# Kernel tuning notes

Measured on AMD Instinct MI355X. Metric: run time of the kernel, lower is better.

The kernel has to match this reference:

```python
import jax, jax.numpy as jnp
import numpy as np

B, TASK, LQ, D = 16, 80, 1024, 768
HH, HD, P, NL = 12, 64, 4, 1
HF, WF = 64, 64
LIN = HF * WF
EPS = 1e-6


def _ln(x, w, b):
    mu = jnp.mean(x, -1, keepdims=True)
    var = jnp.mean(jnp.square(x - mu), -1, keepdims=True)
    return (x - mu) * jax.lax.rsqrt(var + EPS) * w + b


def _bilinear(value_l, loc_l, Hl, Wl):
    # value_l: [B, HH, S, HD]; loc_l: [B, LQ, HH, P, 2] in [0,1]
    # replicates F.grid_sample(align_corners=False, padding_mode='zeros')
    b, hh, s, hd = value_l.shape
    lq, p = loc_l.shape[1], loc_l.shape[3]
    x = loc_l[..., 0] * Wl - 0.5
    y = loc_l[..., 1] * Hl - 0.5
    x0 = jnp.floor(x)
    y0 = jnp.floor(y)
    out = jnp.zeros((b, hh, lq, p, hd), value_l.dtype)
    for dx in (0, 1):
        for dy in (0, 1):
            xc = x0 + dx
            yc = y0 + dy
            w = (1.0 - jnp.abs(x - xc)) * (1.0 - jnp.abs(y - yc))
            valid = (xc >= 0) & (xc <= Wl - 1) & (yc >= 0) & (yc <= Hl - 1)
            w = jnp.where(valid, w, 0.0)
            xi = jnp.clip(xc, 0, Wl - 1).astype(jnp.int32)
            yi = jnp.clip(yc, 0, Hl - 1).astype(jnp.int32)
            lin = (yi * Wl + xi).transpose(0, 2, 1, 3).reshape(b, hh, lq * p, 1)
            v = jnp.take_along_axis(value_l, lin, axis=2).reshape(b, hh, lq, p, hd)
            out = out + v * w.transpose(0, 2, 1, 3)[..., None]
    return out


def _forward(query, reference_points, feat, spatial_shapes, level_start_index,
             qn_w, qn_b, fn_w, fn_b, gamma,
             W_off, b_off, W_attw, b_attw, W_val, b_val, W_out, b_out):
    ss = np.asarray(spatial_shapes)
    lsi = np.asarray(level_start_index)
    tt = query[:, :TASK]
    q = query[:, TASK:]
    bq, lq, _ = q.shape
    qn = _ln(q, qn_w, qn_b)
    fn = _ln(feat, fn_w, fn_b)
    # value projection: [B, Lin, D] -> [B, HH, Lin, HD]
    value = (fn @ W_val + b_val).reshape(bq, -1, HH, HD).transpose(0, 2, 1, 3)
    off = (qn @ W_off + b_off).reshape(bq, lq, HH, NL, P, 2)
    aw = (qn @ W_attw + b_attw).reshape(bq, lq, HH, NL * P)
    aw = jax.nn.softmax(aw, axis=-1).reshape(bq, lq, HH, NL, P)
    # offset normalizer is [W, H] per level
    norm = jnp.stack([ss[:, 1].astype(jnp.float32), ss[:, 0].astype(jnp.float32)], -1)
    loc = reference_points[:, :, None, :, None, :] + off / norm[None, None, None, :, None, :]
    out = jnp.zeros((bq, lq, HH, HD), query.dtype)
    for l in range(ss.shape[0]):
        Hl, Wl = int(ss[l, 0]), int(ss[l, 1])
        st = int(lsi[l])
        vl = value[:, :, st:st + Hl * Wl]
        sampled = _bilinear(vl, loc[:, :, :, l], Hl, Wl)  # [B,HH,LQ,P,HD]
        out = out + jnp.einsum('bhqpd,bqhp->bqhd', sampled, aw[:, :, :, l])
    attn = out.reshape(bq, lq, HH * HD) @ W_out + b_out
    q = q + gamma * attn
    return jnp.concatenate([tt, q], axis=1)


def setup_inputs():
    key = jax.random.key(0)
    ks = jax.random.split(key, 10)
    s = 0.02
    return {
        "query": jax.random.normal(ks[0], (B, TASK + LQ, D), jnp.float32),
        "reference_points": jax.random.uniform(ks[1], (B, LQ, NL, 2), dtype=jnp.float32),
        "feat": jax.random.normal(ks[2], (B, LIN, D), jnp.float32),
        "spatial_shapes": jnp.array([[HF, WF]], jnp.int32),
        "level_start_index": jnp.array([0], jnp.int32),
        "qn_w": jnp.ones((D,), jnp.float32),
        "qn_b": jnp.zeros((D,), jnp.float32),
        "fn_w": jnp.ones((D,), jnp.float32),
        "fn_b": jnp.zeros((D,), jnp.float32),
        "gamma": 0.1 * jax.random.normal(ks[3], (D,), jnp.float32),
        "W_off": s * jax.random.normal(ks[4], (D, HH * NL * P * 2), jnp.float32),
        "b_off": s * jax.random.normal(ks[5], (HH * NL * P * 2,), jnp.float32),
        "W_attw": s * jax.random.normal(ks[6], (D, HH * NL * P), jnp.float32),
        "b_attw": s * jax.random.normal(ks[7], (HH * NL * P,), jnp.float32),
        "W_val": s * jax.random.normal(ks[8], (D, D), jnp.float32),
        "b_val": jnp.zeros((D,), jnp.float32),
        "W_out": s * jax.random.normal(ks[9], (D, D), jnp.float32),
        "b_out": jnp.zeros((D,), jnp.float32),
    }


def reference(query, reference_points, feat, spatial_shapes, level_start_index, qn_w, qn_b, fn_w, fn_b, gamma, W_off, b_off, W_attw, b_attw, W_val, b_val, W_out, b_out):
    return _forward(query, reference_points, feat, spatial_shapes, level_start_index,
                    qn_w, qn_b, fn_w, fn_b, gamma,
                    W_off, b_off, W_attw, b_attw, W_val, b_val, W_out, b_out)
```

## Files before the change

### kernel.cpp

```cpp
#include <hip/hip_runtime.h>
#include <hip/hip_bf16.h>

using bf16 = __hip_bfloat16;
typedef __attribute__((ext_vector_type(8))) short short8;
typedef __attribute__((ext_vector_type(4))) short short4v;
typedef __attribute__((ext_vector_type(4))) float floatx4;

#define B_    16
#define TASK_ 80
#define LQ_   1024
#define D_    768
#define HH_   12
#define HD_   64
#define LIN_  4096
#define MQ_   (B_*LQ_)
#define MF_   (B_*LIN_)
#define QR_   (TASK_+LQ_)

static constexpr size_t OFF_VAL = 0;
static constexpr size_t OFF_FN  = OFF_VAL + (size_t)MF_*D_*2;
static constexpr size_t OFF_QN  = OFF_FN  + (size_t)MF_*D_*2;
static constexpr size_t OFF_OA  = OFF_QN  + (size_t)MQ_*D_*2;
static constexpr size_t OFF_WVT = OFF_OA  + (size_t)MQ_*144*4;
static constexpr size_t OFF_WOT = OFF_WVT + (size_t)D_*D_*2;
static constexpr size_t OFF_WCT = OFF_WOT + (size_t)D_*D_*2;

__device__ __forceinline__ void async16(const void* g, void* l) {
  __builtin_amdgcn_global_load_lds((const __attribute__((address_space(1))) void*)g,
                                   (__attribute__((address_space(3))) void*)l, 16, 0, 0);
}

__global__ __launch_bounds__(256) void k_wln(const float* __restrict__ Wv, const float* __restrict__ Wo,
                                             const float* __restrict__ Woff, const float* __restrict__ Wat,
                                             bf16* __restrict__ WvT, bf16* __restrict__ WoT,
                                             bf16* __restrict__ WcT,
                                             const float* __restrict__ query, const float* __restrict__ feat,
                                             const float* __restrict__ qw, const float* __restrict__ qb,
                                             const float* __restrict__ fw, const float* __restrict__ fb,
                                             bf16* __restrict__ qn, bf16* __restrict__ fn) {
  __shared__ float t[64][65];
  int bid = blockIdx.x;
  if (bid < 288) {
    const float* W = (bid < 144) ? Wv : Wo;
    bf16* WT = (bid < 144) ? WvT : WoT;
    int lb = (bid < 144) ? bid : bid - 144;
    int bx = lb % 12, by = lb / 12;
    int n0 = bx*64, k0 = by*64;
    int col = threadIdx.x & 63, rg = threadIdx.x >> 6;
    #pragma unroll
    for (int i=0;i<16;++i) { int row = i*4+rg; t[row][col] = W[(size_t)(k0+row)*D_ + n0+col]; }
    __syncthreads();
    #pragma unroll
    for (int i=0;i<16;++i) { int row = i*4+rg; WT[(size_t)(n0+row)*D_ + k0+col] = __float2bfloat16(t[col][row]); }
    return;
  }
  if (bid < 1056) {
    int idx = (bid-288)*256 + threadIdx.x;
    int j = idx / D_, k = idx - j*D_;
    float v = 0.f;
    if (j < 96)       v = Woff[(size_t)k*96 + j];
    else if (j < 144) v = Wat[(size_t)k*48 + (j-96)];
    WcT[idx] = __float2bfloat16(v);
    return;
  }
  int r = (bid-1056)*4 + (threadIdx.x>>6);
  int lane = threadIdx.x & 63;
  const float* src; const float* w; const float* bia; bf16* dst;
  if (r < MQ_) {
    int bat = r >> 10, rr = r & 1023;
    src = query + ((size_t)bat*QR_ + TASK_ + rr)*D_;
    w = qw; bia = qb; dst = qn + (size_t)r*D_;
  } else {
    int fr = r - MQ_;
    src = feat + (size_t)fr*D_;
    w = fw; bia = fb; dst = fn + (size_t)fr*D_;
  }
  float4 v[3];
  #pragma unroll
  for (int j=0;j<3;++j) v[j] = ((const float4*)src)[lane + 64*j];
  float s = 0.f, s2 = 0.f;
  #pragma unroll
  for (int j=0;j<3;++j) {
    s  += v[j].x + v[j].y + v[j].z + v[j].w;
    s2 += v[j].x*v[j].x + v[j].y*v[j].y + v[j].z*v[j].z + v[j].w*v[j].w;
  }
  #pragma unroll
  for (int o=32;o>0;o>>=1){ s += __shfl_xor(s,o); s2 += __shfl_xor(s2,o); }
  float mu  = s*(1.f/D_);
  float var = s2*(1.f/D_) - mu*mu;
  float rstd = rsqrtf(var + 1e-6f);
  #pragma unroll
  for (int j=0;j<3;++j) {
    float4 ww = ((const float4*)w)[lane + 64*j];
    float4 bb = ((const float4*)bia)[lane + 64*j];
    short4v o4;
    o4[0] = (short)__bfloat16_as_ushort(__float2bfloat16((v[j].x-mu)*rstd*ww.x + bb.x));
    o4[1] = (short)__bfloat16_as_ushort(__float2bfloat16((v[j].y-mu)*rstd*ww.y + bb.y));
    o4[2] = (short)__bfloat16_as_ushort(__float2bfloat16((v[j].z-mu)*rstd*ww.z + bb.z));
    o4[3] = (short)__bfloat16_as_ushort(__float2bfloat16((v[j].w-mu)*rstd*ww.w + bb.w));
    *(short4v*)(dst + 4*(lane + 64*j)) = o4;
  }
}

template<int MODE>
__global__ __launch_bounds__(512, 2) void k_gemm256(const bf16* __restrict__ A, const bf16* __restrict__ BT,
                                                    const float* __restrict__ bias0, void* __restrict__ outp,
                                                    const float* __restrict__ query, const float* __restrict__ gamma) {
  __shared__ char lds[98304];
  const int K = D_;
  const int tid = threadIdx.x, wid = tid>>6, lane = tid&63;
  const int nwg = gridDim.x*gridDim.y;
  const int d = blockIdx.y*gridDim.x + blockIdx.x;
  const int logical = (d & 7)*(nwg>>3) + (d>>3);
  const int bm = (logical/3)*256, bn = (logical%3)*256;
  const int wm = wid>>2, wn = wid&3;
  const int srow = tid>>2;
  const int sslot = ((tid&3) ^ ((tid>>3)&3))*8;
  const bf16* gA0 = A  + (size_t)(bm + srow)*K + sslot;
  const bf16* gA1 = A  + (size_t)(bm + 128 + srow)*K + sslot;
  const bf16* gB0 = BT + (size_t)(bn + srow)*K + sslot;
  const bf16* gB1 = BT + (size_t)(bn + 128 + srow)*K + sslot;
  const int dstbase = (tid>>6)<<10;
  const int rb = (lane&15)*64 + ((((lane>>4) ^ ((lane>>1)&3)))<<4);
  floatx4 acc[8][4] = {};
  auto stageAll = [&](int k0, char* buf) {
    async16(gA0+k0, buf + dstbase);
    async16(gA1+k0, buf + 8192 + dstbase);
    async16(gB0+k0, buf + 16384 + dstbase);
    async16(gB1+k0, buf + 24576 + dstbase);
  };
  stageAll(0,  lds);
  stageAll(32, lds + 32768);
  const int NT = K >> 5;
  int cur = 0, nxt = 2;
  for (int k = 0; k < NT; ++k) {
    if (k < NT-1) asm volatile("s_waitcnt vmcnt(4)" ::: "memory");
    else          asm volatile("s_waitcnt vmcnt(0)" ::: "memory");
    __builtin_amdgcn_s_barrier();
    __builtin_amdgcn_sched_barrier(0);
    const int kk = (k+2)*32;
    const bool pf = (k+2 < NT);
    const char* lA = lds + cur*32768;
    const char* lB = lA + 16384;
    char* bufn = lds + nxt*32768;
    short8 af[8], bfr[4];
    if (pf) async16(gA0+kk, bufn + dstbase);
    #pragma unroll
    for (int i=0;i<4;++i) af[i] = *(const short8*)(lA + (wm*128 + i*16)*64 + rb);
    #pragma unroll
    for (int i=0;i<2;++i) bfr[i] = *(const short8*)(lB + (wn*64 + i*16)*64 + rb);
    __builtin_amdgcn_s_barrier();
    __builtin_amdgcn_s_setprio(1);
    #pragma unroll
    for (int mi=0;mi<4;++mi)
      #pragma unroll
      for (int ni=0;ni<2;++ni)
        acc[mi][ni] = __builtin_amdgcn_mfma_f32_16x16x32_bf16(af[mi], bfr[ni], acc[mi][ni], 0, 0, 0);
    __builtin_amdgcn_s_setprio(0);
    __builtin_amdgcn_s_barrier();
    __builtin_amdgcn_sched_barrier(0);
    if (pf) async16(gA1+kk, bufn + 8192 + dstbase);
    #pragma unroll
    for (int i=2;i<4;++i) bfr[i] = *(const short8*)(lB + (wn*64 + i*16)*64 + rb);
    __builtin_amdgcn_s_barrier();
    __builtin_amdgcn_s_setprio(1);
    #pragma unroll
    for (int mi=0;mi<4;++mi)
      #pragma unroll
      for (int ni=2;ni<4;++ni)
        acc[mi][ni] = __builtin_amdgcn_mfma_f32_16x16x32_bf16(af[mi], bfr[ni], acc[mi][ni], 0, 0, 0);
    __builtin_amdgcn_s_setprio(0);
    __builtin_amdgcn_s_barrier();
    __builtin_amdgcn_sched_barrier(0);
    if (pf) async16(gB0+kk, bufn + 16384 + dstbase);
    #pragma unroll
    for (int i=4;i<8;++i) af[i] = *(const short8*)(lA + (wm*128 + i*16)*64 + rb);
    __builtin_amdgcn_s_barrier();
    __builtin_amdgcn_s_setprio(1);
    #pragma unroll
    for (int mi=4;mi<8;++mi)
      #pragma unroll
      for (int ni=0;ni<2;++ni)
        acc[mi][ni] = __builtin_amdgcn_mfma_f32_16x16x32_bf16(af[mi], bfr[ni], acc[mi][ni], 0, 0, 0);
    __builtin_amdgcn_s_setprio(0);
    __builtin_amdgcn_s_barrier();
    __builtin_amdgcn_sched_barrier(0);
    if (pf) async16(gB1+kk, bufn + 24576 + dstbase);
    __builtin_amdgcn_s_barrier();
    __builtin_amdgcn_s_setprio(1);
    #pragma unroll
    for (int mi=4;mi<8;++mi)
      #pragma unroll
      for (int ni=2;ni<4;++ni)
        acc[mi][ni] = __builtin_amdgcn_mfma_f32_16x16x32_bf16(af[mi], bfr[ni], acc[mi][ni], 0, 0, 0);
    __builtin_amdgcn_s_setprio(0);
    __builtin_amdgcn_sched_barrier(0);
    cur = (cur==2) ? 0 : cur+1;
    nxt = (nxt==2) ? 0 : nxt+1;
  }
  const int rowb = (lane>>4)*4, col = lane&15;
  #pragma unroll
  for (int mi=0;mi<8;++mi) {
    #pragma unroll
    for (int ni=0;ni<4;++ni) {
      const int gn = bn + wn*64 + ni*16 + col;
      const float bv = bias0[gn];
      #pragma unroll
      for (int r=0;r<4;++r) {
        const int gm = bm + wm*128 + mi*16 + rowb + r;
        if constexpr (MODE==0) {
          const int h = gn >> 6, hd = gn & 63;
          const int b = gm >> 12, pix = gm & 4095;
          ((bf16*)outp)[(((size_t)(b*HH_+h)*LIN_ + pix)<<6) + hd] = __float2bfloat16(acc[mi][ni][r] + bv);
        } else {
          const int bq = gm >> 10, lq = gm & 1023;
          size_t idx = ((size_t)bq*QR_ + TASK_ + lq)*D_ + gn;
          ((float*)outp)[idx] = query[idx] + gamma[gn]*(acc[mi][ni][r] + bv);
        }
      }
    }
  }
}

__global__ __launch_bounds__(256) void k_gemm1(const bf16* __restrict__ A, const bf16* __restrict__ BT,
                                               int K,
                                               const float* __restrict__ bias0, const float* __restrict__ bias1,
                                               float* __restrict__ outp) {
  __shared__ char lds[49152];
  const int tid = threadIdx.x, wid = tid>>6, lane = tid&63;
  const int nwg = gridDim.x*gridDim.y, ny = gridDim.y;
  const int d = blockIdx.y*gridDim.x + blockIdx.x;
  const int logical = (d & 7)*(nwg>>3) + (d>>3);
  const int bm = (logical/ny)*128, bn = (logical%ny)*128;
  const int wr = wid>>1, wc = wid&1;
  const int c0 = wid*2, c1 = c0+1;
  const int sr0 = c0*16 + (lane>>2), sr1 = sr0+16;
  const int skb = (((lane&3) ^ ((lane>>3)&3)))*8;
  const bf16* ga0 = A  + (size_t)(bm+sr0)*K + skb;
  const bf16* ga1 = A  + (size_t)(bm+sr1)*K + skb;
  const bf16* gb0 = BT + (size_t)(bn+sr0)*K + skb;
  const bf16* gb1 = BT + (size_t)(bn+sr1)*K + skb;
  const int rb = (lane&15)*64 + ((((lane>>4) ^ ((lane>>1)&3)))<<4);
  floatx4 acc[4][4] = {};
  auto stage = [&](int k0, char* buf) {
    char* dA = buf; char* dB = buf + 8192;
    async16(ga0+k0, dA + c0*1024); async16(ga1+k0, dA + c1*1024);
    async16(gb0+k0, dB + c0*1024); async16(gb1+k0, dB + c1*1024);
  };
  stage(0,  lds);
  stage(32, lds + 16384);
  const int NT = K >> 5;
  int cur = 0, nxt = 2;
  for (int k = 0; k < NT; ++k) {
    if (k < NT-1) asm volatile("s_waitcnt vmcnt(4)" ::: "memory");
    else          asm volatile("s_waitcnt vmcnt(0)" ::: "memory");
    __builtin_amdgcn_s_barrier();
    __builtin_amdgcn_sched_barrier(0);
    if (k + 2 < NT) stage((k+2)*32, lds + nxt*16384);
    const char* ldsA = lds + cur*16384; const char* ldsB = ldsA + 8192;
    short8 af[4], bfr[4];
    #pragma unroll
    for (int i=0;i<4;++i) {
      af[i]  = *(const short8*)(ldsA + (wr*64 + i*16)*64 + rb);
      bfr[i] = *(const short8*)(ldsB + (wc*64 + i*16)*64 + rb);
    }
    #pragma unroll
    for (int mi=0;mi<4;++mi)
      #pragma unroll
      for (int ni=0;ni<4;++ni)
        acc[mi][ni] = __builtin_amdgcn_mfma_f32_16x16x32_bf16(af[mi], bfr[ni], acc[mi][ni], 0, 0, 0);
    cur = (cur==2) ? 0 : cur+1;
    nxt = (nxt==2) ? 0 : nxt+1;
  }
  const int rowb = (lane>>4)*4, col = lane&15;
  #pragma unroll
  for (int mi=0;mi<4;++mi) {
    #pragma unroll
    for (int ni=0;ni<4;++ni) {
      const int gn = bn + wc*64 + ni*16 + col;
      #pragma unroll
      for (int r=0;r<4;++r) {
        const int gm = bm + wr*64 + mi*16 + rowb + r;
        float v = acc[mi][ni][r];
        if (gn < 144) {
          v += (gn < 96) ? bias0[gn] : bias1[gn-96];
          outp[(size_t)gm*144 + gn] = v;
        }
      }
    }
  }
}

__global__ __launch_bounds__(256) void k_prep(const float* __restrict__ oa_all,
                                              const float* __restrict__ refp,
                                              float2* __restrict__ prep,
                                              const float* __restrict__ query, float* __restrict__ out) {
  int idx = blockIdx.x*256 + threadIdx.x;
  int p = idx & 3, mh = idx >> 2;
  int h = mh % HH_, m = mh / HH_;
  const float* oa = oa_all + (size_t)m*144;
  float l0 = oa[96+h*4+0], l1 = oa[96+h*4+1], l2 = oa[96+h*4+2], l3 = oa[96+h*4+3];
  float mx = fmaxf(fmaxf(l0,l1), fmaxf(l2,l3));
  float e0 = expf(l0-mx), e1 = expf(l1-mx), e2 = expf(l2-mx), e3 = expf(l3-mx);
  float inv = 1.f/(e0+e1+e2+e3);
  float ep = (p==0)?e0:(p==1)?e1:(p==2)?e2:e3;
  float awp = ep*inv;
  float x = refp[(size_t)m*2+0]*64.f - 0.5f + oa[h*8+p*2+0];
  float y = refp[(size_t)m*2+1]*64.f - 0.5f + oa[h*8+p*2+1];
  float x0f = floorf(x), y0f = floorf(y);
  int ix = (int)x0f, iy = (int)y0f;
  float fx = x-x0f, fy = y-y0f;
  float wx[2] = {1.f-fx, fx}, wy[2] = {1.f-fy, fy};
  float2 e[4];
  #pragma unroll
  for (int c=0;c<4;++c) {
    int dx = c&1, dy = c>>1;
    int xc = ix+dx, yc = iy+dy;
    bool valid = ((unsigned)xc < 64u) && ((unsigned)yc < 64u);
    float w = valid ? awp*wx[dx]*wy[dy] : 0.f;
    int xi = min(max(xc,0),63), yi = min(max(yc,0),63);
    e[c].x = w;
    e[c].y = __int_as_float(yi*64+xi);
  }
  float2* dst = prep + (size_t)mh*16 + p*4;
  *(float4*)(dst)   = make_float4(e[0].x, e[0].y, e[1].x, e[1].y);
  *(float4*)(dst+2) = make_float4(e[2].x, e[2].y, e[3].x, e[3].y);
  if (blockIdx.x < 960) {
    int ci = blockIdx.x*256 + threadIdx.x;
    const int perb = TASK_*D_/4;
    int b = ci / perb, r = ci - b*perb;
    const float4* s = (const float4*)(query + (size_t)b*QR_*D_) + r;
    float4* dd = (float4*)(out + (size_t)b*QR_*D_) + r;
    *dd = *s;
  }
}

__global__ __launch_bounds__(256) void k_sample(const float2* __restrict__ prep,
                                                const bf16* __restrict__ value,
                                                bf16* __restrict__ sampout) {
  int g  = blockIdx.x*8 + (threadIdx.x>>5);
  int l  = threadIdx.x & 31;
  int c8 = l >> 2, p = l & 3;
  int h = g % HH_, m = g / HH_;
  int b = m >> 10;
  const float2* pb = prep + (size_t)g*16 + p*4;
  float4 e01 = *(const float4*)(pb);
  float4 e23 = *(const float4*)(pb+2);
  const bf16* vb = value + (((size_t)(b*HH_+h))<<18) + (c8<<3);
  float a[8] = {};
  float wv[4]  = {e01.x, e01.z, e23.x, e23.z};
  int   pix[4] = {__float_as_int(e01.y), __float_as_int(e01.w),
                  __float_as_int(e23.y), __float_as_int(e23.w)};
  #pragma unroll
  for (int c=0;c<4;++c) {
    short8 v = *(const short8*)(vb + ((size_t)pix[c]<<6));
    float w = wv[c];
    #pragma unroll
    for (int j=0;j<8;++j)
      a[j] += w*__uint_as_float(((unsigned)(unsigned short)v[j])<<16);
  }
  #pragma unroll
  for (int j=0;j<8;++j) { a[j] += __shfl_xor(a[j],1); a[j] += __shfl_xor(a[j],2); }
  if (p == 0) {
    short8 o;
    #pragma unroll
    for (int j=0;j<8;++j)
      o[j] = (short)__bfloat16_as_ushort(__float2bfloat16(a[j]));
    *(short8*)(sampout + (size_t)m*D_ + h*64 + c8*8) = o;
  }
}

extern "C" void kernel_launch(void* const* d_in, const int* in_sizes, int n_in,
                              void* d_out, int out_size, void* d_ws, size_t ws_size,
                              hipStream_t stream) {
  (void)in_sizes; (void)n_in; (void)out_size; (void)ws_size;
  const float* query = (const float*)d_in[0];
  const float* refp  = (const float*)d_in[1];
  const float* feat  = (const float*)d_in[2];
  const float* qn_w  = (const float*)d_in[5];
  const float* qn_b  = (const float*)d_in[6];
  const float* fn_w  = (const float*)d_in[7];
  const float* fn_b  = (const float*)d_in[8];
  const float* gamma = (const float*)d_in[9];
  const float* W_off = (const float*)d_in[10];
  const float* b_off = (const float*)d_in[11];
  const float* W_attw= (const float*)d_in[12];
  const float* b_attw= (const float*)d_in[13];
  const float* W_val = (const float*)d_in[14];
  const float* b_val = (const float*)d_in[15];
  const float* W_out = (const float*)d_in[16];
  const float* b_out = (const float*)d_in[17];
  char*  ws  = (char*)d_ws;
  float* out = (float*)d_out;

  bf16*   wsVal  = (bf16*)(ws + OFF_VAL);
  bf16*   wsFn   = (bf16*)(ws + OFF_FN);
  bf16*   wsQn   = (bf16*)(ws + OFF_QN);
  float*  wsOA   = (float*)(ws + OFF_OA);
  bf16*   wsWvT  = (bf16*)(ws + OFF_WVT);
  bf16*   wsWoT  = (bf16*)(ws + OFF_WOT);
  bf16*   wsWcT  = (bf16*)(ws + OFF_WCT);
  float2* wsPrep = (float2*)(ws + OFF_QN);
  bf16*   wsSamp = wsFn;

  k_wln<<<1056 + (MQ_+MF_)/4, 256, 0, stream>>>(W_val, W_out, W_off, W_attw, wsWvT, wsWoT, wsWcT,
                                                query, feat, qn_w, qn_b, fn_w, fn_b, wsQn, wsFn);
  k_gemm1<<<dim3(MQ_/128, 2), 256, 0, stream>>>(wsQn, wsWcT, D_, b_off, b_attw, wsOA);
  k_prep<<<(MQ_*HH_*4)/256, 256, 0, stream>>>(wsOA, refp, wsPrep, query, out);
  k_gemm256<0><<<dim3(MF_/256, 3), 512, 0, stream>>>(wsFn, wsWvT, b_val, wsVal, nullptr, nullptr);
  k_sample<<<(MQ_*HH_)/8, 256, 0, stream>>>(wsPrep, wsVal, wsSamp);
  k_gemm256<2><<<dim3(MQ_/256, 3), 512, 0, stream>>>(wsSamp, wsWoT, b_out, out, query, gamma);
}
```

Measured before the change: 276.2 us.

## Fuse offset/attention GEMM with sampling prep and pack prep data as bf16/u16

New measurement: 269.2 us. 1.03x faster.

```diff
diff --git a/kernel.cpp b/kernel.cpp
--- a/kernel.cpp
+++ b/kernel.cpp
@@ -17,13 +17,13 @@
 #define MF_   (B_*LIN_)
 #define QR_   (TASK_+LQ_)
 
-static constexpr size_t OFF_VAL = 0;
-static constexpr size_t OFF_FN  = OFF_VAL + (size_t)MF_*D_*2;
-static constexpr size_t OFF_QN  = OFF_FN  + (size_t)MF_*D_*2;
-static constexpr size_t OFF_OA  = OFF_QN  + (size_t)MQ_*D_*2;
-static constexpr size_t OFF_WVT = OFF_OA  + (size_t)MQ_*144*4;
-static constexpr size_t OFF_WOT = OFF_WVT + (size_t)D_*D_*2;
-static constexpr size_t OFF_WCT = OFF_WOT + (size_t)D_*D_*2;
+static constexpr size_t OFF_VAL  = 0;
+static constexpr size_t OFF_FN   = OFF_VAL + (size_t)MF_*D_*2;
+static constexpr size_t OFF_QN   = OFF_FN  + (size_t)MF_*D_*2;
+static constexpr size_t OFF_PREP = OFF_QN  + (size_t)MQ_*D_*2;
+static constexpr size_t OFF_WVT  = OFF_PREP + (size_t)MQ_*HH_*64;
+static constexpr size_t OFF_WOT  = OFF_WVT + (size_t)D_*D_*2;
+static constexpr size_t OFF_WCT  = OFF_WOT + (size_t)D_*D_*2;
 
 __device__ __forceinline__ void async16(const void* g, void* l) {
   __builtin_amdgcn_global_load_lds((const __attribute__((address_space(1))) void*)g,
@@ -99,6 +99,118 @@
     o4[2] = (short)__bfloat16_as_ushort(__float2bfloat16((v[j].z-mu)*rstd*ww.z + bb.z));
     o4[3] = (short)__bfloat16_as_ushort(__float2bfloat16((v[j].w-mu)*rstd*ww.w + bb.w));
     *(short4v*)(dst + 4*(lane + 64*j)) = o4;
+  }
+}
+
+__global__ __launch_bounds__(256) void k_offprep(const bf16* __restrict__ A, const bf16* __restrict__ BT,
+                                                 const float* __restrict__ b_off, const float* __restrict__ b_attw,
+                                                 const float* __restrict__ refp, char* __restrict__ prepc,
+                                                 const float* __restrict__ query, float* __restrict__ out) {
+  __shared__ char lds[49152];
+  const int tid = threadIdx.x, wid = tid>>6, lane = tid&63;
+  const int bm = blockIdx.x*64;
+  const int K = D_;
+  const int srow = tid>>2;
+  const int skb = ((tid&3) ^ ((tid>>3)&3))*8;
+  const bf16* gA  = A  + (size_t)(bm + srow)*K + skb;
+  const bf16* gB  = BT + (size_t)srow*K + skb;
+  const int dstbase = wid<<10;
+  const int rb = (lane&15)*64 + ((((lane>>4) ^ ((lane>>1)&3)))<<4);
+  floatx4 acc[4][3] = {};
+  auto stage = [&](int k0, char* buf) {
+    async16(gA + k0,                 buf + dstbase);
+    async16(gB + k0,                 buf + 4096  + dstbase);
+    async16(gB + (size_t)64*K + k0,  buf + 8192  + dstbase);
+    async16(gB + (size_t)128*K + k0, buf + 12288 + dstbase);
+  };
+  stage(0,  lds);
+  stage(32, lds + 16384);
+  const int NT = K >> 5;
+  int cur = 0, nxt = 2;
+  for (int k = 0; k < NT; ++k) {
+    if (k < NT-1) asm volatile("s_waitcnt vmcnt(4)" ::: "memory");
+    else          asm volatile("s_waitcnt vmcnt(0)" ::: "memory");
+    __builtin_amdgcn_s_barrier();
+    __builtin_amdgcn_sched_barrier(0);
+    if (k + 2 < NT) stage((k+2)*32, lds + nxt*16384);
+    const char* ldsA = lds + cur*16384; const char* ldsB = ldsA + 4096;
+    short8 af[4], bf[3];
+    #pragma unroll
+    for (int i=0;i<4;++i) af[i] = *(const short8*)(ldsA + (i*16)*64 + rb);
+    #pragma unroll
+    for (int j=0;j<3;++j) bf[j] = *(const short8*)(ldsB + (wid*48 + j*16)*64 + rb);
+    #pragma unroll
+    for (int mi=0;mi<4;++mi)
+      #pragma unroll
+      for (int ni=0;ni<3;++ni)
+        acc[mi][ni] = __builtin_amdgcn_mfma_f32_16x16x32_bf16(af[mi], bf[ni], acc[mi][ni], 0, 0, 0);
+    cur = (cur==2) ? 0 : cur+1;
+    nxt = (nxt==2) ? 0 : nxt+1;
+  }
+  __syncthreads();
+  float* oa = (float*)lds;
+  const int rowb = (lane>>4)*4, col = lane&15;
+  #pragma unroll
+  for (int mi=0;mi<4;++mi) {
+    #pragma unroll
+    for (int ni=0;ni<3;++ni) {
+      const int gn = wid*48 + ni*16 + col;
+      if (gn < 144) {
+        const float bv = (gn < 96) ? b_off[gn] : b_attw[gn-96];
+        #pragma unroll
+        for (int r=0;r<4;++r) {
+          const int rl = mi*16 + rowb + r;
+          oa[rl*148 + gn] = acc[mi][ni][r] + bv;
+        }
+      }
+    }
+  }
+  __syncthreads();
+  #pragma unroll
+  for (int i=0;i<12;++i) {
+    int item = tid + i*256;
+    int rl = item / 48;
+    int hp = item - rl*48;
+    int h = hp >> 2, p = hp & 3;
+    int m = bm + rl;
+    const float* row = oa + rl*148;
+    float l0 = row[96+h*4+0], l1 = row[96+h*4+1], l2 = row[96+h*4+2], l3 = row[96+h*4+3];
+    float mx = fmaxf(fmaxf(l0,l1), fmaxf(l2,l3));
+    float e0 = expf(l0-mx), e1 = expf(l1-mx), e2 = expf(l2-mx), e3 = expf(l3-mx);
+    float inv = 1.f/(e0+e1+e2+e3);
+    float ep = (p==0)?e0:(p==1)?e1:(p==2)?e2:e3;
+    float awp = ep*inv;
+    float x = refp[(size_t)m*2+0]*64.f - 0.5f + row[h*8+p*2+0];
+    float y = refp[(size_t)m*2+1]*64.f - 0.5f + row[h*8+p*2+1];
+    float x0f = floorf(x), y0f = floorf(y);
+    int ix = (int)x0f, iy = (int)y0f;
+    float fx = x-x0f, fy = y-y0f;
+    float wx[2] = {1.f-fx, fx}, wy[2] = {1.f-fy, fy};
+    short4v wq, pq;
+    #pragma unroll
+    for (int c=0;c<4;++c) {
+      int dx = c&1, dy = c>>1;
+      int xc = ix+dx, yc = iy+dy;
+      bool valid = ((unsigned)xc < 64u) && ((unsigned)yc < 64u);
+      float w = valid ? awp*wx[dx]*wy[dy] : 0.f;
+      int xi = min(max(xc,0),63), yi = min(max(yc,0),63);
+      wq[c] = (short)__bfloat16_as_ushort(__float2bfloat16(w));
+      pq[c] = (short)(yi*64+xi);
+    }
+    char* gb = prepc + ((size_t)(m*HH_ + h))*64;
+    *(short4v*)(gb + p*8)      = wq;
+    *(short4v*)(gb + 32 + p*8) = pq;
+  }
+  #pragma unroll
+  for (int i=0;i<4;++i) {
+    int ci = blockIdx.x*256 + tid + i*65536;
+    if (ci < B_*TASK_*D_/4) {
+      const int perb = TASK_*D_/4;
+      int b = ci / perb, r = ci - b*perb;
+      const float4* s = (const float4*)(query + (size_t)b*QR_*D_) + r;
+      float4* dd = (float4*)(out + (size_t)b*QR_*D_) + r;
+      *dd = *s;
+    }
   }
 }
 
@@ -222,120 +334,7 @@
   }
 }
 
-__global__ __launch_bounds__(256) void k_gemm1(const bf16* __restrict__ A, const bf16* __restrict__ BT,
-                                               int K,
-                                               const float* __restrict__ bias0, const float* __restrict__ bias1,
-                                               float* __restrict__ outp) {
-  __shared__ char lds[49152];
-  const int tid = threadIdx.x, wid = tid>>6, lane = tid&63;
-  const int nwg = gridDim.x*gridDim.y, ny = gridDim.y;
-  const int d = blockIdx.y*gridDim.x + blockIdx.x;
-  const int logical = (d & 7)*(nwg>>3) + (d>>3);
-  const int bm = (logical/ny)*128, bn = (logical%ny)*128;
-  const int wr = wid>>1, wc = wid&1;
-  const int c0 = wid*2, c1 = c0+1;
-  const int sr0 = c0*16 + (lane>>2), sr1 = sr0+16;
-  const int skb = (((lane&3) ^ ((lane>>3)&3)))*8;
-  const bf16* ga0 = A  + (size_t)(bm+sr0)*K + skb;
-  const bf16* ga1 = A  + (size_t)(bm+sr1)*K + skb;
-  const bf16* gb0 = BT + (size_t)(bn+sr0)*K + skb;
-  const bf16* gb1 = BT + (size_t)(bn+sr1)*K + skb;
-  const int rb = (lane&15)*64 + ((((lane>>4) ^ ((lane>>1)&3)))<<4);
-  floatx4 acc[4][4] = {};
-  auto stage = [&](int k0, char* buf) {
-    char* dA = buf; char* dB = buf + 8192;
-    async16(ga0+k0, dA + c0*1024); async16(ga1+k0, dA + c1*1024);
-    async16(gb0+k0, dB + c0*1024); async16(gb1+k0, dB + c1*1024);
-  };
-  stage(0,  lds);
-  stage(32, lds + 16384);
-  const int NT = K >> 5;
-  int cur = 0, nxt = 2;
-  for (int k = 0; k < NT; ++k) {
-    if (k < NT-1) asm volatile("s_waitcnt vmcnt(4)" ::: "memory");
-    else          asm volatile("s_waitcnt vmcnt(0)" ::: "memory");
-    __builtin_amdgcn_s_barrier();
-    __builtin_amdgcn_sched_barrier(0);
-    if (k + 2 < NT) stage((k+2)*32, lds + nxt*16384);
-    const char* ldsA = lds + cur*16384; const char* ldsB = ldsA + 8192;
-    short8 af[4], bfr[4];
-    #pragma unroll
-    for (int i=0;i<4;++i) {
-      af[i]  = *(const short8*)(ldsA + (wr*64 + i*16)*64 + rb);
-      bfr[i] = *(const short8*)(ldsB + (wc*64 + i*16)*64 + rb);
-    }
-    #pragma unroll
-    for (int mi=0;mi<4;++mi)
-      #pragma unroll
-      for (int ni=0;ni<4;++ni)
-        acc[mi][ni] = __builtin_amdgcn_mfma_f32_16x16x32_bf16(af[mi], bfr[ni], acc[mi][ni], 0, 0, 0);
-    cur = (cur==2) ? 0 : cur+1;
-    nxt = (nxt==2) ? 0 : nxt+1;
-  }
-  const int rowb = (lane>>4)*4, col = lane&15;
-  #pragma unroll
-  for (int mi=0;mi<4;++mi) {
-    #pragma unroll
-    for (int ni=0;ni<4;++ni) {
-      const int gn = bn + wc*64 + ni*16 + col;
-      #pragma unroll
-      for (int r=0;r<4;++r) {
-        const int gm = bm + wr*64 + mi*16 + rowb + r;
-        float v = acc[mi][ni][r];
-        if (gn < 144) {
-          v += (gn < 96) ? bias0[gn] : bias1[gn-96];
-          outp[(size_t)gm*144 + gn] = v;
-        }
-      }
-    }
-  }
-}
-
-__global__ __launch_bounds__(256) void k_prep(const float* __restrict__ oa_all,
-                                              const float* __restrict__ refp,
-                                              float2* __restrict__ prep,
-                                              const float* __restrict__ query, float* __restrict__ out) {
-  int idx = blockIdx.x*256 + threadIdx.x;
-  int p = idx & 3, mh = idx >> 2;
-  int h = mh % HH_, m = mh / HH_;
-  const float* oa = oa_all + (size_t)m*144;
-  float l0 = oa[96+h*4+0], l1 = oa[96+h*4+1], l2 = oa[96+h*4+2], l3 = oa[96+h*4+3];
-  float mx = fmaxf(fmaxf(l0,l1), fmaxf(l2,l3));
-  float e0 = expf(l0-mx), e1 = expf(l1-mx), e2 = expf(l2-mx), e3 = expf(l3-mx);
-  float inv = 1.f/(e0+e1+e2+e3);
-  float ep = (p==0)?e0:(p==1)?e1:(p==2)?e2:e3;
-  float awp = ep*inv;
-  float x = refp[(size_t)m*2+0]*64.f - 0.5f + oa[h*8+p*2+0];
-  float y = refp[(size_t)m*2+1]*64.f - 0.5f + oa[h*8+p*2+1];
-  float x0f = floorf(x), y0f = floorf(y);
-  int ix = (int)x0f, iy = (int)y0f;
-  float fx = x-x0f, fy = y-y0f;
-  float wx[2] = {1.f-fx, fx}, wy[2] = {1.f-fy, fy};
-  float2 e[4];
-  #pragma unroll
-  for (int c=0;c<4;++c) {
-    int dx = c&1, dy = c>>1;
-    int xc = ix+dx, yc = iy+dy;
-    bool valid = ((unsigned)xc < 64u) && ((unsigned)yc < 64u);
-    float w = valid ? awp*wx[dx]*wy[dy] : 0.f;
-    int xi = min(max(xc,0),63), yi = min(max(yc,0),63);
-    e[c].x = w;
-    e[c].y = __int_as_float(yi*64+xi);
-  }
-  float2* dst = prep + (size_t)mh*16 + p*4;
-  *(float4*)(dst)   = make_float4(e[0].x, e[0].y, e[1].x, e[1].y);
-  *(float4*)(dst+2) = make_float4(e[2].x, e[2].y, e[3].x, e[3].y);
-  if (blockIdx.x < 960) {
-    int ci = blockIdx.x*256 + threadIdx.x;
-    const int perb = TASK_*D_/4;
-    int b = ci / perb, r = ci - b*perb;
-    const float4* s = (const float4*)(query + (size_t)b*QR_*D_) + r;
-    float4* dd = (float4*)(out + (size_t)b*QR_*D_) + r;
-    *dd = *s;
-  }
-}
-
-__global__ __launch_bounds__(256) void k_sample(const float2* __restrict__ prep,
+__global__ __launch_bounds__(256) void k_sample(const char* __restrict__ prepc,
                                                 const bf16* __restrict__ value,
                                                 bf16* __restrict__ sampout) {
   int g  = blockIdx.x*8 + (threadIdx.x>>5);
@@ -343,18 +342,16 @@
   int c8 = l >> 2, p = l & 3;
   int h = g % HH_, m = g / HH_;
   int b = m >> 10;
-  const float2* pb = prep + (size_t)g*16 + p*4;
-  float4 e01 = *(const float4*)(pb);
-  float4 e23 = *(const float4*)(pb+2);
+  const char* gb = prepc + (size_t)g*64;
+  short4v wq = *(const short4v*)(gb + p*8);
+  short4v pq = *(const short4v*)(gb + 32 + p*8);
   const bf16* vb = value + (((size_t)(b*HH_+h))<<18) + (c8<<3);
   float a[8] = {};
-  float wv[4]  = {e01.x, e01.z, e23.x, e23.z};
-  int   pix[4] = {__float_as_int(e01.y), __float_as_int(e01.w),
-                  __float_as_int(e23.y), __float_as_int(e23.w)};
   #pragma unroll
   for (int c=0;c<4;++c) {
-    short8 v = *(const short8*)(vb + ((size_t)pix[c]<<6));
-    float w = wv[c];
+    float w = __uint_as_float(((unsigned)(unsigned short)wq[c])<<16);
+    int pix = (int)(unsigned short)pq[c];
+    short8 v = *(const short8*)(vb + ((size_t)pix<<6));
     #pragma unroll
     for (int j=0;j<8;++j)
       a[j] += w*__uint_as_float(((unsigned)(unsigned short)v[j])<<16);
@@ -393,20 +390,18 @@
   char*  ws  = (char*)d_ws;
   float* out = (float*)d_out;
 
-  bf16*   wsVal  = (bf16*)(ws + OFF_VAL);
-  bf16*   wsFn   = (bf16*)(ws + OFF_FN);
-  bf16*   wsQn   = (bf16*)(ws + OFF_QN);
-  float*  wsOA   = (float*)(ws + OFF_OA);
-  bf16*   wsWvT  = (bf16*)(ws + OFF_WVT);
-  bf16*   wsWoT  = (bf16*)(ws + OFF_WOT);
-  bf16*   wsWcT  = (bf16*)(ws + OFF_WCT);
-  float2* wsPrep = (float2*)(ws + OFF_QN);
-  bf16*   wsSamp = wsFn;
+  bf16* wsVal  = (bf16*)(ws + OFF_VAL);
+  bf16* wsFn   = (bf16*)(ws + OFF_FN);
+  bf16* wsQn   = (bf16*)(ws + OFF_QN);
+  char* wsPrep = ws + OFF_PREP;
+  bf16* wsWvT  = (bf16*)(ws + OFF_WVT);
+  bf16* wsWoT  = (bf16*)(ws + OFF_WOT);
+  bf16* wsWcT  = (bf16*)(ws + OFF_WCT);
+  bf16* wsSamp = wsFn;
 
   k_wln<<<1056 + (MQ_+MF_)/4, 256, 0, stream>>>(W_val, W_out, W_off, W_attw, wsWvT, wsWoT, wsWcT,
                                                 query, feat, qn_w, qn_b, fn_w, fn_b, wsQn, wsFn);
-  k_gemm1<<<dim3(MQ_/128, 2), 256, 0, stream>>>(wsQn, wsWcT, D_, b_off, b_attw, wsOA);
-  k_prep<<<(MQ_*HH_*4)/256, 256, 0, stream>>>(wsOA, refp, wsPrep, query, out);
+  k_offprep<<<MQ_/64, 256, 0, stream>>>(wsQn, wsWcT, b_off, b_attw, refp, wsPrep, query, out);
   k_gemm256<0><<<dim3(MF_/256, 3), 512, 0, stream>>>(wsFn, wsWvT, b_val, wsVal, nullptr, nullptr);
   k_sample<<<(MQ_*HH_)/8, 256, 0, stream>>>(wsPrep, wsVal, wsSamp);
   k_gemm256<2><<<dim3(MQ_/256, 3), 512, 0, stream>>>(wsSamp, wsWoT, b_out, out, query, gamma);
```
